# Kernel tuning notes

Measured on AMD Instinct MI355X. Metric: run time of the kernel, lower is better.

The kernel has to match this reference:

```python
import jax, jax.numpy as jnp
import numpy as np
import math

# Module hyperparameters (from init_kwargs)
T_TOTAL = 1.0
NUM_STEPS = 8          # == len(F), number of time-indexed sub-networks (experts)
D = 1024               # feature dim (shape = [D])
DH = 4096              # hidden dim of each expert MLP
B = 4096               # batch size
H_STEP = T_TOTAL / NUM_STEPS
EIGMIN, EIGINIT, EIGMAX = -1.0, 0.0, 1.0   # spectral_limits=None
INV_SIG_099 = math.log(0.99 / (1 - 0.99))  # shifta/shiftb/scales init (learn flags False)


def setup_inputs() -> dict:
    key = jax.random.key(0)
    ks = jax.random.split(key, 8)
    t = jax.random.uniform(ks[0], (B,), dtype=jnp.float32) * T_TOTAL
    y = jax.random.normal(ks[1], (B, D), dtype=jnp.float32)
    # Per-expert 2-layer MLP params, stacked over the expert axis E
    s1 = 1.0 / math.sqrt(D)
    s2 = 1.0 / math.sqrt(DH)
    W1 = jax.random.normal(ks[2], (NUM_STEPS, D, DH), dtype=jnp.float32) * s1
    b1 = jnp.zeros((NUM_STEPS, DH), dtype=jnp.float32)
    W2 = jax.random.normal(ks[3], (NUM_STEPS, DH, D), dtype=jnp.float32) * s2
    b2 = jnp.zeros((NUM_STEPS, D), dtype=jnp.float32)
    scales = jnp.full((1, D), INV_SIG_099, dtype=jnp.float32)
    shifta = jnp.float32(INV_SIG_099)
    shiftb = jnp.float32(INV_SIG_099)
    return {"t": t, "y": y, "W1": W1, "b1": b1, "W2": W2, "b2": b2,
            "scales": scales, "shifta": shifta, "shiftb": shiftb}


def reference(t, y, W1, b1, W2, b2, scales, shifta, shiftb):
    E = W1.shape[0]
    # t2ind: per-sample expert index, clamped to the last expert
    ind = jnp.minimum((t / H_STEP).astype(jnp.int32), E - 1)          # [B]
    # Run every expert on every sample (dense dispatch), then gather per-sample result.
    hid = jnp.tanh(jnp.einsum('bd,edh->ebh', y, W1) + b1[:, None, :])  # [E,B,DH]
    fe = jnp.einsum('ebh,ehd->ebd', hid, W2) + b2[:, None, :]          # [E,B,D]
    f = jnp.take_along_axis(fe, ind[None, :, None].astype(jnp.int32), axis=0)[0]  # [B,D]
    f = jax.nn.sigmoid(scales) * f
    a = EIGINIT + jax.nn.sigmoid(shifta) * (EIGMIN - EIGINIT)
    b = EIGINIT + jax.nn.sigmoid(shiftb) * (EIGMAX - EIGINIT)
    return 0.5 * ((b - a) * f + (a + b) * y)
```

## Files before the change

kernel.cpp:

```cpp
#include <hip/hip_runtime.h>
#include <hip/hip_bf16.h>
#include <math.h>

#define NEXP 8
#define DIM_D 1024
#define DIM_H 4096
#define NB 4096

typedef __attribute__((ext_vector_type(8))) short short8;
typedef __attribute__((ext_vector_type(4))) float floatx4;

__device__ __forceinline__ unsigned short f2bf(float x) {
  __hip_bfloat16 h = __float2bfloat16(x);
  unsigned short u;
  __builtin_memcpy(&u, &h, 2);
  return u;
}
__device__ __forceinline__ unsigned int pack2bf(float a, float b) {
  return (unsigned int)f2bf(a) | ((unsigned int)f2bf(b) << 16);
}

__device__ __forceinline__ void async_copy16(const void* g, void* l) {
  __builtin_amdgcn_global_load_lds(
      (const __attribute__((address_space(1))) unsigned int*)g,
      (__attribute__((address_space(3))) unsigned int*)l, 16, 0, 0);
}

__global__ void setup_kernel(const float* __restrict__ t,
                             int* __restrict__ offs, int* __restrict__ perm,
                             int* __restrict__ wl) {
  __shared__ int cnt[NEXP];
  __shared__ int cur[NEXP];
  const int tid = threadIdx.x;
  if (tid < NEXP) cnt[tid] = 0;
  __syncthreads();
  for (int i = tid; i < NB; i += 256) {
    int e = (int)(t[i] * 8.0f);
    e = e < 0 ? 0 : (e > NEXP - 1 ? NEXP - 1 : e);
    atomicAdd(&cnt[e], 1);
  }
  __syncthreads();
  if (tid == 0) {
    int s = 0;
    for (int e = 0; e < NEXP; ++e) { offs[e] = s; cur[e] = s; s += cnt[e]; }
    offs[NEXP] = s;
    for (int i = 0; i < 64; ++i) wl[i] = -1;
    for (int e = 0; e < NEXP; ++e) {
      int tiles = (cnt[e] + 127) >> 7;
      int lim = tiles < 8 ? tiles : 8;
      for (int r = 0; r < lim; ++r) wl[r * 8 + e] = (r << 4) | e;
    }
    int free_s = 0;
    for (int e = 0; e < NEXP; ++e) {
      int tiles = (cnt[e] + 127) >> 7;
      for (int r = 8; r < tiles; ++r) {
        while (free_s < 64 && wl[free_s] >= 0) ++free_s;
        if (free_s < 64) wl[free_s] = (r << 4) | e;
      }
    }
  }
  __syncthreads();
  for (int i = tid; i < NB; i += 256) {
    int e = (int)(t[i] * 8.0f);
    e = e < 0 ? 0 : (e > NEXP - 1 ? NEXP - 1 : e);
    int slot = atomicAdd(&cur[e], 1);
    perm[slot] = i;
  }
}

__global__ __launch_bounds__(256)
void cvt_kernel(const float* __restrict__ in, __hip_bfloat16* __restrict__ out) {
  const long long i = ((long long)blockIdx.x * 256 + threadIdx.x) * 8;
  const float4 a = *(const float4*)(in + i);
  const float4 b = *(const float4*)(in + i + 4);
  unsigned int r[4];
  r[0] = pack2bf(a.x, a.y);
  r[1] = pack2bf(a.z, a.w);
  r[2] = pack2bf(b.x, b.y);
  r[3] = pack2bf(b.z, b.w);
  *(uint4*)(out + i) = *(const uint4*)r;
}

__global__ __launch_bounds__(256)
void transpose_cvt_kernel(const float* __restrict__ in,
                          __hip_bfloat16* __restrict__ out, int R, int C) {
  __shared__ unsigned int wbuf[32 * 69];
  const long long base = (long long)blockIdx.z * R * C;
  const int c0 = blockIdx.x * 64;
  const int r0 = blockIdx.y * 64;
  const int t = threadIdx.x;
  {
    const int p = t >> 3, g = t & 7;
    const float* s0 = in + base + (long long)(r0 + 2 * p) * C + c0 + g * 8;
    const float4 a0 = *(const float4*)(s0);
    const float4 a1 = *(const float4*)(s0 + 4);
    const float4 b0 = *(const float4*)(s0 + C);
    const float4 b1v = *(const float4*)(s0 + C + 4);
    unsigned int* dp = &wbuf[p * 69 + g * 8];
    dp[0] = pack2bf(a0.x, b0.x);
    dp[1] = pack2bf(a0.y, b0.y);
    dp[2] = pack2bf(a0.z, b0.z);
    dp[3] = pack2bf(a0.w, b0.w);
    dp[4] = pack2bf(a1.x, b1v.x);
    dp[5] = pack2bf(a1.y, b1v.y);
    dp[6] = pack2bf(a1.z, b1v.z);
    dp[7] = pack2bf(a1.w, b1v.w);
  }
  __syncthreads();
  {
    const int oc = t >> 2, rq = t & 3;
    __align__(16) unsigned int res[8];
#pragma unroll
    for (int j = 0; j < 8; ++j) res[j] = wbuf[(rq * 8 + j) * 69 + oc];
    __hip_bfloat16* dstp = out + base + (long long)(c0 + oc) * R + r0 + rq * 16;
    *(uint4*)dstp = *(const uint4*)&res[0];
    *(uint4*)(dstp + 8) = *(const uint4*)&res[4];
  }
}

template <int MODE>
__global__ __launch_bounds__(256, 2)
void gemm_kernel(const __hip_bfloat16* __restrict__ A,
                 const __hip_bfloat16* __restrict__ BT,
                 const float* __restrict__ bias,
                 const int* __restrict__ offs, const int* __restrict__ perm,
                 const int* __restrict__ wl,
                 void* __restrict__ dstv,
                 const float* __restrict__ yin,
                 const float* __restrict__ scales,
                 const float* __restrict__ shifta,
                 const float* __restrict__ shiftb,
                 int K, int N) {
  const int wle = wl[blockIdx.y];
  if (wle < 0) return;
  const int e  = wle & 15;
  const int mt = wle >> 4;
  const int off = offs[e];
  const int cnt = offs[e + 1] - off;
  const int m0 = mt * 128;
  if (m0 >= cnt) return;
  const int rows = min(128, cnt - m0);
  const int n0 = blockIdx.x * 128;

  __shared__ __align__(16) char lds[65536];
  __shared__ int rowmap[128];

  const int tid = threadIdx.x;
  if (tid < 128) {
    int r = tid < rows ? tid : rows - 1;
    rowmap[tid] = (MODE == 0) ? perm[off + m0 + r] : (off + m0 + r);
  }
  __syncthreads();

  const int w = tid >> 6, l = tid & 63;

  const int q_s = ((tid >> 2) & 3) ^ ((tid >> 4) & 3);
  const int kc  = (tid & 3) ^ q_s;
  const int r2  = tid >> 2;
  const __hip_bfloat16* aptr[2];
  const __hip_bfloat16* bptr[2];
#pragma unroll
  for (int i = 0; i < 2; ++i) {
    const int row = i * 64 + r2;
    aptr[i] = A + (long long)rowmap[row] * K + kc * 8;
    bptr[i] = BT + ((long long)e * N + n0 + row) * K + kc * 8;
  }

  auto stage = [&](int buf) {
    char* dst = lds + (buf << 14);
#pragma unroll
    for (int i = 0; i < 2; ++i) {
      async_copy16(aptr[i], dst + i * 4096 + w * 1024);
      async_copy16(bptr[i], dst + 8192 + i * 4096 + w * 1024);
      aptr[i] += 32; bptr[i] += 32;
    }
  };

  floatx4 acc[4][4];
#pragma unroll
  for (int i = 0; i < 4; ++i)
#pragma unroll
    for (int j = 0; j < 4; ++j) acc[i][j] = (floatx4){0.f, 0.f, 0.f, 0.f};

  const int wm = w >> 1, wn = w & 1;
  const int fr = l & 15;
  const int fq = l >> 4;
  const int slot = fq ^ ((fr & 3) ^ ((fr >> 2) & 3));
  const unsigned lbase = (unsigned)(unsigned long long)
      (__attribute__((address_space(3))) char*)lds;
  const unsigned abase = lbase + (unsigned)((wm * 64 + fr) * 64 + slot * 16);
  const unsigned bbase = lbase + 8192u + (unsigned)((wn * 64 + fr) * 64 + slot * 16);

  auto compute = [&](int buf) {
    const unsigned ab = abase + (unsigned)(buf << 14);
    const unsigned bb = bbase + (unsigned)(buf << 14);
    short8 af0, af1, af2, af3, bf0, bf1, bf2, bf3;
    asm volatile("ds_read_b128 %0, %1" : "=v"(af0) : "v"(ab));
    asm volatile("ds_read_b128 %0, %1 offset:1024" : "=v"(af1) : "v"(ab));
    asm volatile("ds_read_b128 %0, %1 offset:2048" : "=v"(af2) : "v"(ab));
    asm volatile("ds_read_b128 %0, %1 offset:3072" : "=v"(af3) : "v"(ab));
    asm volatile("ds_read_b128 %0, %1" : "=v"(bf0) : "v"(bb));
    asm volatile("ds_read_b128 %0, %1 offset:1024" : "=v"(bf1) : "v"(bb));
    asm volatile("ds_read_b128 %0, %1 offset:2048" : "=v"(bf2) : "v"(bb));
    asm volatile("ds_read_b128 %0, %1 offset:3072" : "=v"(bf3) : "v"(bb));
    asm volatile("s_waitcnt lgkmcnt(0)" ::: "memory");
    __builtin_amdgcn_sched_barrier(0);
    short8 af[4] = {af0, af1, af2, af3};
    short8 bf[4] = {bf0, bf1, bf2, bf3};
#pragma unroll
    for (int mi = 0; mi < 4; ++mi)
#pragma unroll
      for (int ni = 0; ni < 4; ++ni)
        acc[mi][ni] = __builtin_amdgcn_mfma_f32_16x16x32_bf16(
            af[mi], bf[ni], acc[mi][ni], 0, 0, 0);
  };

  const int nt = K >> 5;

  stage(0); stage(1); stage(2);

  int t = 0;
  for (; t < nt - 3; ++t) {
    asm volatile("s_waitcnt vmcnt(8)" ::: "memory");
    __builtin_amdgcn_s_barrier();
    stage((t + 3) & 3);
    compute(t & 3);
  }
  asm volatile("s_waitcnt vmcnt(8)" ::: "memory");
  __builtin_amdgcn_s_barrier();
  compute(t & 3); ++t;
  asm volatile("s_waitcnt vmcnt(4)" ::: "memory");
  __builtin_amdgcn_s_barrier();
  compute(t & 3); ++t;
  asm volatile("s_waitcnt vmcnt(0)" ::: "memory");
  __builtin_amdgcn_s_barrier();
  compute(t & 3);

  float av = 0.f, bv = 0.f;
  if (MODE == 1) {
    const float sa = 1.f / (1.f + expf(-shifta[0]));
    const float sb = 1.f / (1.f + expf(-shiftb[0]));
    av = 0.0f + sa * (-1.0f - 0.0f);
    bv = 0.0f + sb * (1.0f - 0.0f);
  }

#pragma unroll
  for (int mi = 0; mi < 4; ++mi) {
#pragma unroll
    for (int r = 0; r < 4; ++r) {
      const int rl = wm * 64 + mi * 16 + fq * 4 + r;
      if (rl >= rows) continue;
      const int i = off + m0 + rl;
      const int orig = (MODE == 1) ? perm[i] : 0;
#pragma unroll
      for (int ni = 0; ni < 4; ++ni) {
        const int cg = n0 + wn * 64 + ni * 16 + fr;
        const float x = acc[mi][ni][r] + bias[e * N + cg];
        if (MODE == 0) {
          ((__hip_bfloat16*)dstv)[(long long)i * N + cg] = __float2bfloat16(tanhf(x));
        } else {
          const float sc = 1.f / (1.f + expf(-scales[cg]));
          const float yv = yin[(long long)orig * N + cg];
          const float res = 0.5f * ((bv - av) * sc * x + (av + bv) * yv);
          ((float*)dstv)[(long long)orig * N + cg] = res;
        }
      }
    }
  }
}

extern "C" void kernel_launch(void* const* d_in, const int* in_sizes, int n_in,
                              void* d_out, int out_size, void* d_ws, size_t ws_size,
                              hipStream_t stream) {
  const float* t      = (const float*)d_in[0];
  const float* y      = (const float*)d_in[1];
  const float* W1     = (const float*)d_in[2];
  const float* b1     = (const float*)d_in[3];
  const float* W2     = (const float*)d_in[4];
  const float* b2     = (const float*)d_in[5];
  const float* scales = (const float*)d_in[6];
  const float* shifta = (const float*)d_in[7];
  const float* shiftb = (const float*)d_in[8];

  char* ws = (char*)d_ws;
  __hip_bfloat16* WT  = (__hip_bfloat16*)ws;
  __hip_bfloat16* hid = (__hip_bfloat16*)(ws + (size_t)64 * 1024 * 1024);
  __hip_bfloat16* ybf = (__hip_bfloat16*)(ws + (size_t)96 * 1024 * 1024);
  int* offs = (int*)(ws + (size_t)104 * 1024 * 1024);
  int* perm = offs + 16;
  int* wl   = perm + NB;

  setup_kernel<<<1, 256, 0, stream>>>(t, offs, perm, wl);

  cvt_kernel<<<(NB * DIM_D) / (256 * 8), 256, 0, stream>>>(y, ybf);

  transpose_cvt_kernel<<<dim3(DIM_H / 64, DIM_D / 64, NEXP), 256, 0, stream>>>(
      W1, WT, DIM_D, DIM_H);
  gemm_kernel<0><<<dim3(DIM_H / 128, 64), 256, 0, stream>>>(
      ybf, WT, b1, offs, perm, wl, hid, nullptr, nullptr, nullptr, nullptr,
      DIM_D, DIM_H);
  transpose_cvt_kernel<<<dim3(DIM_D / 64, DIM_H / 64, NEXP), 256, 0, stream>>>(
      W2, WT, DIM_H, DIM_D);
  gemm_kernel<1><<<dim3(DIM_D / 128, 64), 256, 0, stream>>>(
      hid, WT, b2, offs, perm, wl, d_out, y, scales, shifta, shiftb,
      DIM_H, DIM_D);
}
```

Before: 505.3 us.

## Double GEMM K-tile to 64 with new swizzle and swap grid axes

Each pipeline stage in the GEMM now loads a 64-wide K slice instead of 32, so LDS grows to 128KB and occupancy drops to one block per CU. The XOR swizzle is redone for 128-byte rows. LDS reads are split into two halves so the MFMAs on the first half overlap the outstanding reads of the second. The grid axes are swapped so consecutive blocks walk work-list tiles and share a weight N-tile. The work-list setup is also parallelised across threads. The aim is to halve barriers per K and improve weight reuse in L2, at the cost of losing the latency hiding from two resident blocks.

```diff
diff --git a/kernel.cpp b/kernel.cpp
--- a/kernel.cpp
+++ b/kernel.cpp
@@ -44,12 +44,15 @@
     int s = 0;
     for (int e = 0; e < NEXP; ++e) { offs[e] = s; cur[e] = s; s += cnt[e]; }
     offs[NEXP] = s;
-    for (int i = 0; i < 64; ++i) wl[i] = -1;
-    for (int e = 0; e < NEXP; ++e) {
-      int tiles = (cnt[e] + 127) >> 7;
-      int lim = tiles < 8 ? tiles : 8;
-      for (int r = 0; r < lim; ++r) wl[r * 8 + e] = (r << 4) | e;
-    }
+  }
+  __syncthreads();
+  if (tid < 64) {
+    const int r = tid >> 3, e = tid & 7;
+    const int tiles = (cnt[e] + 127) >> 7;
+    wl[tid] = (r < tiles) ? ((r << 4) | e) : -1;
+  }
+  __syncthreads();
+  if (tid == 0) {
     int free_s = 0;
     for (int e = 0; e < NEXP; ++e) {
       int tiles = (cnt[e] + 127) >> 7;
@@ -59,7 +62,6 @@
       }
     }
   }
-  __syncthreads();
   for (int i = tid; i < NB; i += 256) {
     int e = (int)(t[i] * 8.0f);
     e = e < 0 ? 0 : (e > NEXP - 1 ? NEXP - 1 : e);
@@ -119,7 +121,7 @@
 }
 
 template <int MODE>
-__global__ __launch_bounds__(256, 2)
+__global__ __launch_bounds__(256, 1)
 void gemm_kernel(const __hip_bfloat16* __restrict__ A,
                  const __hip_bfloat16* __restrict__ BT,
                  const float* __restrict__ bias,
@@ -131,7 +133,7 @@
                  const float* __restrict__ shifta,
                  const float* __restrict__ shiftb,
                  int K, int N) {
-  const int wle = wl[blockIdx.y];
+  const int wle = wl[blockIdx.x];
   if (wle < 0) return;
   const int e  = wle & 15;
   const int mt = wle >> 4;
@@ -140,9 +142,9 @@
   const int m0 = mt * 128;
   if (m0 >= cnt) return;
   const int rows = min(128, cnt - m0);
-  const int n0 = blockIdx.x * 128;
-
-  __shared__ __align__(16) char lds[65536];
+  const int n0 = blockIdx.y * 128;
+
+  __shared__ __align__(16) char lds[131072];
   __shared__ int rowmap[128];
 
   const int tid = threadIdx.x;
@@ -154,25 +156,24 @@
 
   const int w = tid >> 6, l = tid & 63;
 
-  const int q_s = ((tid >> 2) & 3) ^ ((tid >> 4) & 3);
-  const int kc  = (tid & 3) ^ q_s;
-  const int r2  = tid >> 2;
-  const __hip_bfloat16* aptr[2];
-  const __hip_bfloat16* bptr[2];
-#pragma unroll
-  for (int i = 0; i < 2; ++i) {
-    const int row = i * 64 + r2;
-    aptr[i] = A + (long long)rowmap[row] * K + kc * 8;
-    bptr[i] = BT + ((long long)e * N + n0 + row) * K + kc * 8;
+  const int srow = tid >> 3;
+  const int kc = (tid & 7) ^ (srow & 7);
+  const __hip_bfloat16* aptr[4];
+  const __hip_bfloat16* bptr[4];
+#pragma unroll
+  for (int j = 0; j < 4; ++j) {
+    const int row = j * 32 + srow;
+    aptr[j] = A + (long long)rowmap[row] * K + kc * 8;
+    bptr[j] = BT + ((long long)e * N + n0 + row) * K + kc * 8;
   }
 
   auto stage = [&](int buf) {
-    char* dst = lds + (buf << 14);
-#pragma unroll
-    for (int i = 0; i < 2; ++i) {
-      async_copy16(aptr[i], dst + i * 4096 + w * 1024);
-      async_copy16(bptr[i], dst + 8192 + i * 4096 + w * 1024);
-      aptr[i] += 32; bptr[i] += 32;
+    char* dst = lds + (buf << 15);
+#pragma unroll
+    for (int j = 0; j < 4; ++j) {
+      async_copy16(aptr[j], dst + j * 4096 + w * 1024);
+      async_copy16(bptr[j], dst + 16384 + j * 4096 + w * 1024);
+      aptr[j] += 64; bptr[j] += 64;
     }
   };
 
@@ -185,51 +186,74 @@
   const int wm = w >> 1, wn = w & 1;
   const int fr = l & 15;
   const int fq = l >> 4;
-  const int slot = fq ^ ((fr & 3) ^ ((fr >> 2) & 3));
   const unsigned lbase = (unsigned)(unsigned long long)
       (__attribute__((address_space(3))) char*)lds;
-  const unsigned abase = lbase + (unsigned)((wm * 64 + fr) * 64 + slot * 16);
-  const unsigned bbase = lbase + 8192u + (unsigned)((wn * 64 + fr) * 64 + slot * 16);
+  const unsigned aks0 = lbase + (unsigned)((wm * 64 + fr) * 128 +
+                                           ((fq ^ (fr & 7)) << 4));
+  const unsigned bks0 = aks0 + 16384u + (unsigned)(((wn - wm) * 64) * 128);
+  const unsigned aks1 = aks0 ^ 64u;
+  const unsigned bks1 = bks0 ^ 64u;
 
   auto compute = [&](int buf) {
-    const unsigned ab = abase + (unsigned)(buf << 14);
-    const unsigned bb = bbase + (unsigned)(buf << 14);
-    short8 af0, af1, af2, af3, bf0, bf1, bf2, bf3;
-    asm volatile("ds_read_b128 %0, %1" : "=v"(af0) : "v"(ab));
-    asm volatile("ds_read_b128 %0, %1 offset:1024" : "=v"(af1) : "v"(ab));
-    asm volatile("ds_read_b128 %0, %1 offset:2048" : "=v"(af2) : "v"(ab));
-    asm volatile("ds_read_b128 %0, %1 offset:3072" : "=v"(af3) : "v"(ab));
-    asm volatile("ds_read_b128 %0, %1" : "=v"(bf0) : "v"(bb));
-    asm volatile("ds_read_b128 %0, %1 offset:1024" : "=v"(bf1) : "v"(bb));
-    asm volatile("ds_read_b128 %0, %1 offset:2048" : "=v"(bf2) : "v"(bb));
-    asm volatile("ds_read_b128 %0, %1 offset:3072" : "=v"(bf3) : "v"(bb));
+    const unsigned bo = (unsigned)(buf << 15);
+    const unsigned a0 = aks0 + bo, a1 = aks1 + bo;
+    const unsigned b0 = bks0 + bo, b1 = bks1 + bo;
+    short8 A0, A1, A2, A3, B0, B1, B2, B3;
+    short8 C0, C1, C2, C3, D0, D1, D2, D3;
+    asm volatile("ds_read_b128 %0, %1" : "=v"(A0) : "v"(a0));
+    asm volatile("ds_read_b128 %0, %1 offset:2048" : "=v"(A1) : "v"(a0));
+    asm volatile("ds_read_b128 %0, %1 offset:4096" : "=v"(A2) : "v"(a0));
+    asm volatile("ds_read_b128 %0, %1 offset:6144" : "=v"(A3) : "v"(a0));
+    asm volatile("ds_read_b128 %0, %1" : "=v"(B0) : "v"(b0));
+    asm volatile("ds_read_b128 %0, %1 offset:2048" : "=v"(B1) : "v"(b0));
+    asm volatile("ds_read_b128 %0, %1 offset:4096" : "=v"(B2) : "v"(b0));
+    asm volatile("ds_read_b128 %0, %1 offset:6144" : "=v"(B3) : "v"(b0));
+    asm volatile("ds_read_b128 %0, %1" : "=v"(C0) : "v"(a1));
+    asm volatile("ds_read_b128 %0, %1 offset:2048" : "=v"(C1) : "v"(a1));
+    asm volatile("ds_read_b128 %0, %1 offset:4096" : "=v"(C2) : "v"(a1));
+    asm volatile("ds_read_b128 %0, %1 offset:6144" : "=v"(C3) : "v"(a1));
+    asm volatile("ds_read_b128 %0, %1" : "=v"(D0) : "v"(b1));
+    asm volatile("ds_read_b128 %0, %1 offset:2048" : "=v"(D1) : "v"(b1));
+    asm volatile("ds_read_b128 %0, %1 offset:4096" : "=v"(D2) : "v"(b1));
+    asm volatile("ds_read_b128 %0, %1 offset:6144" : "=v"(D3) : "v"(b1));
+    asm volatile("s_waitcnt lgkmcnt(8)" ::: "memory");
+    __builtin_amdgcn_sched_barrier(0);
+    {
+      short8 af[4] = {A0, A1, A2, A3};
+      short8 bf[4] = {B0, B1, B2, B3};
+#pragma unroll
+      for (int mi = 0; mi < 4; ++mi)
+#pragma unroll
+        for (int ni = 0; ni < 4; ++ni)
+          acc[mi][ni] = __builtin_amdgcn_mfma_f32_16x16x32_bf16(
+              af[mi], bf[ni], acc[mi][ni], 0, 0, 0);
+    }
     asm volatile("s_waitcnt lgkmcnt(0)" ::: "memory");
     __builtin_amdgcn_sched_barrier(0);
-    short8 af[4] = {af0, af1, af2, af3};
-    short8 bf[4] = {bf0, bf1, bf2, bf3};
-#pragma unroll
-    for (int mi = 0; mi < 4; ++mi)
-#pragma unroll
-      for (int ni = 0; ni < 4; ++ni)
-        acc[mi][ni] = __builtin_amdgcn_mfma_f32_16x16x32_bf16(
-            af[mi], bf[ni], acc[mi][ni], 0, 0, 0);
+    {
+      short8 af[4] = {C0, C1, C2, C3};
+      short8 bf[4] = {D0, D1, D2, D3};
+#pragma unroll
+      for (int mi = 0; mi < 4; ++mi)
+#pragma unroll
+        for (int ni = 0; ni < 4; ++ni)
+          acc[mi][ni] = __builtin_amdgcn_mfma_f32_16x16x32_bf16(
+              af[mi], bf[ni], acc[mi][ni], 0, 0, 0);
+    }
   };
 
-  const int nt = K >> 5;
+  const int nt = K >> 6;
 
   stage(0); stage(1); stage(2);
 
   int t = 0;
-  for (; t < nt - 3; ++t) {
-    asm volatile("s_waitcnt vmcnt(8)" ::: "memory");
+  for (; t < nt - 2; ++t) {
+    asm volatile("s_waitcnt vmcnt(16)" ::: "memory");
     __builtin_amdgcn_s_barrier();
-    stage((t + 3) & 3);
+    if (t + 3 < nt) stage((t + 3) & 3);
     compute(t & 3);
   }
   asm volatile("s_waitcnt vmcnt(8)" ::: "memory");
-  __builtin_amdgcn_s_barrier();
-  compute(t & 3); ++t;
-  asm volatile("s_waitcnt vmcnt(4)" ::: "memory");
   __builtin_amdgcn_s_barrier();
   compute(t & 3); ++t;
   asm volatile("s_waitcnt vmcnt(0)" ::: "memory");
@@ -296,12 +320,12 @@
 
   transpose_cvt_kernel<<<dim3(DIM_H / 64, DIM_D / 64, NEXP), 256, 0, stream>>>(
       W1, WT, DIM_D, DIM_H);
-  gemm_kernel<0><<<dim3(DIM_H / 128, 64), 256, 0, stream>>>(
+  gemm_kernel<0><<<dim3(64, DIM_H / 128), 256, 0, stream>>>(
       ybf, WT, b1, offs, perm, wl, hid, nullptr, nullptr, nullptr, nullptr,
       DIM_D, DIM_H);
   transpose_cvt_kernel<<<dim3(DIM_D / 64, DIM_H / 64, NEXP), 256, 0, stream>>>(
       W2, WT, DIM_H, DIM_D);
-  gemm_kernel<1><<<dim3(DIM_D / 128, 64), 256, 0, stream>>>(
+  gemm_kernel<1><<<dim3(64, DIM_D / 128), 256, 0, stream>>>(
       hid, WT, b2, offs, perm, wl, d_out, y, scales, shifta, shiftb,
       DIM_H, DIM_D);
 }
```

New measurement: 608.0 us. 1.2x slower.
